# Optimization experiments

Hardware: AMD Instinct MI355X
Metric: run time of the kernel (lower is better)

The kernel has to match this reference:

```python
import jax, jax.numpy as jnp
import numpy as np

N, E, H, R, A = 100000, 1600000, 128, 500, 16  # nodes, edges, hidden, reservoir, actions
LN_EPS = 1e-5

def setup_inputs() -> dict:
    key = jax.random.key(0)
    ks = jax.random.split(key, 8)
    return {
        "node_feats": jax.random.normal(ks[0], (N, 2), jnp.float32),
        "edge_index": jax.random.randint(ks[1], (2, E), 0, N, dtype=jnp.int32),
        "esn_state": jax.random.normal(ks[2], (1, R), jnp.float32),
        "gcn_w": jax.random.normal(ks[3], (2, H), jnp.float32) * 0.5,
        "gcn_b": jnp.zeros((H,), jnp.float32),
        "ln_w": jnp.ones((H,), jnp.float32),
        "ln_b": jnp.zeros((H,), jnp.float32),
        "fc1_w": jax.random.normal(ks[4], (H + R, H), jnp.float32) * 0.04,
        "fc1_b": jnp.zeros((H,), jnp.float32),
        "fc2_w": jax.random.normal(ks[5], (H, A), jnp.float32) * 0.08,
        "fc2_b": jnp.zeros((A,), jnp.float32),
    }

def reference(node_feats, edge_index, esn_state, gcn_w, gcn_b, ln_w, ln_b,
              fc1_w, fc1_b, fc2_w, fc2_b):
    src, dst = edge_index[0], edge_index[1]
    n = node_feats.shape[0]
    # GCNConv: linear transform, then symmetric-normalized aggregation with self-loops
    h = node_feats @ gcn_w  # [N, H]
    deg = jax.ops.segment_sum(jnp.ones_like(src, dtype=h.dtype), dst, num_segments=n) + 1.0
    dis = jax.lax.rsqrt(deg)  # deg >= 1 due to self-loops
    norm = dis[src] * dis[dst]  # [E]
    agg = jax.ops.segment_sum(h[src] * norm[:, None], dst, num_segments=n)  # [N, H]
    x = agg + h * (dis * dis)[:, None] + gcn_b  # self-loop term + bias
    x = jax.nn.relu(x)
    # PyG LayerNorm, mode='graph', batch=None: normalize over all nodes & channels
    x = x - x.mean()
    x = x / (jnp.sqrt(x.var()) + LN_EPS)
    x = x * ln_w + ln_b
    pooled = x.sum(axis=0, keepdims=True)  # global_add_pool, single graph -> [1, H]
    z = jnp.concatenate([pooled, esn_state], axis=1)  # [1, H+R]
    z = jax.nn.relu(z @ fc1_w + fc1_b)
    logits = z @ fc2_w + fc2_b  # [1, A]
    return jax.nn.log_softmax(logits, axis=1)
```

## Files before the change

kernel.cpp:

```cpp
#include <hip/hip_runtime.h>
#include <math.h>

#define NN 100000
#define EE 1600000
#define HH 128
#define RR 500
#define AA 16
#define LN_EPS 1e-5f

#define BSH 8
#define NPB 256
#define NB 391
#define MAXPB 4608
#define EPW 8192
#define SCT 512
#define NWG_SC ((EE + EPW - 1) / EPW)
#define NZW 16
#define BAT 512
#define NSREP 8
#define NTW 16

__global__ __launch_bounds__(256) void k_init_esn(unsigned int* __restrict__ zero_region,
                                                  const float* __restrict__ esn,
                                                  const float* __restrict__ fc1_w,
                                                  float* __restrict__ zpart) {
    const int w = blockIdx.x, t = threadIdx.x;
    if (w == 0) {
        for (int j = t; j < 1544; j += 256) zero_region[j] = 0u;
        return;
    }
    const int sl = w - 1;
    const int k0 = sl * 32;
    const int k1 = min(k0 + 32, RR);
    if (t < HH) {
        float acc = 0.f;
        for (int k = k0; k < k1; ++k)
            acc = fmaf(esn[k], fc1_w[(size_t)(HH + k) * HH + t], acc);
        zpart[(size_t)sl * HH + t] = acc;
    }
}

__global__ __launch_bounds__(SCT) void k_scatter(const int* __restrict__ src,
                                                 const int* __restrict__ dst,
                                                 unsigned int* __restrict__ gctr,
                                                 unsigned int* __restrict__ payload) {
    __shared__ unsigned int rank[512], hbase[512];
    const int t = threadIdx.x;
    rank[t] = 0u; hbase[t] = 0u;
    __syncthreads();
    const int e0 = blockIdx.x * EPW;
    const int ecnt = max(0, min(EPW, EE - e0));
    const int nv = ecnt >> 2;
    const int4* d4 = reinterpret_cast<const int4*>(dst + e0);
    const int4* s4 = reinterpret_cast<const int4*>(src + e0);

    unsigned int pw[16], pbr[16];
    bool vk[4];

    #pragma unroll
    for (int kk = 0; kk < 4; ++kk) {
        const int k = t + kk * SCT;
        vk[kk] = (k < nv);
        if (vk[kk]) {
            int4 d = d4[k];
            int4 s = s4[k];
            #define GRAB(i, SS, DD) { \
                unsigned int dd = (unsigned)(DD), ss = (unsigned)(SS); \
                unsigned int b = dd >> BSH; \
                unsigned int r = atomicAdd(&rank[b], 1u); \
                pw[kk * 4 + i]  = (ss << BSH) | (dd & (NPB - 1)); \
                pbr[kk * 4 + i] = (b << 16) | (r & 0xFFFFu); }
            GRAB(0, s.x, d.x) GRAB(1, s.y, d.y) GRAB(2, s.z, d.z) GRAB(3, s.w, d.w)
            #undef GRAB
        }
    }
    __syncthreads();

    if (t < NB && rank[t] > 0u) hbase[t] = atomicAdd(&gctr[t], rank[t]);
    __syncthreads();

    #pragma unroll
    for (int kk = 0; kk < 4; ++kk) {
        if (vk[kk]) {
            #define PUT(i) { \
                unsigned int b = pbr[kk * 4 + i] >> 16; \
                unsigned int slot = hbase[b] + (pbr[kk * 4 + i] & 0xFFFFu); \
                if (slot < MAXPB) payload[(size_t)b * MAXPB + slot] = pw[kk * 4 + i]; }
            PUT(0) PUT(1) PUT(2) PUT(3)
            #undef PUT
        }
    }
}

__global__ __launch_bounds__(1024) void k_bdeg_g(const unsigned int* __restrict__ gctr,
                                                 const unsigned int* __restrict__ payload,
                                                 const float* __restrict__ nf,
                                                 float* __restrict__ rsv, float* __restrict__ g) {
    __shared__ unsigned int hist[NPB];
    const int b = blockIdx.x, t = threadIdx.x;
    if (t < NPB) hist[t] = 0u;
    __syncthreads();
    const unsigned int cnt = min(gctr[b], (unsigned int)MAXPB);
    const unsigned int* pl = payload + (size_t)b * MAXPB;
    const uint4* pl4 = reinterpret_cast<const uint4*>(pl);
    const unsigned int nv = cnt >> 2;
    for (unsigned int k = t; k < nv; k += 1024) {
        uint4 p = pl4[k];
        atomicAdd(&hist[p.x & (NPB - 1)], 1u);
        atomicAdd(&hist[p.y & (NPB - 1)], 1u);
        atomicAdd(&hist[p.z & (NPB - 1)], 1u);
        atomicAdd(&hist[p.w & (NPB - 1)], 1u);
    }
    for (unsigned int k = (nv << 2) + t; k < cnt; k += 1024)
        atomicAdd(&hist[pl[k] & (NPB - 1)], 1u);
    __syncthreads();
    if (t < NPB) {
        int node = (b << BSH) + t;
        if (node < NN) {
            float df = 1.0f + (float)hist[t];
            float rs = rsqrtf(df);
            rsv[node] = rs;
            float2 f = *reinterpret_cast<const float2*>(&nf[2 * node]);
            float2 gv; gv.x = rs * f.x; gv.y = rs * f.y;
            *reinterpret_cast<float2*>(&g[2 * node]) = gv;
        }
    }
}

__global__ __launch_bounds__(BAT) void k_bagg_node(const unsigned int* __restrict__ gctr,
        const unsigned int* __restrict__ payload,
        const float* __restrict__ g, const float* __restrict__ rsv,
        const float* __restrict__ gcn_w, const float* __restrict__ gcn_b,
        float* __restrict__ S8, float* __restrict__ T2_8) {
    __shared__ float agg[NPB * 2];
    __shared__ float shSf[HH];
    __shared__ float shw[8];
    const int b = blockIdx.x, t = threadIdx.x;
    agg[t] = 0.f;
    if (t < HH) shSf[t] = 0.f;
    __syncthreads();
    const unsigned int cnt = min(gctr[b], (unsigned int)MAXPB);
    const unsigned int* pl = payload + (size_t)b * MAXPB;
    const uint4* pl4 = reinterpret_cast<const uint4*>(pl);
    const unsigned int nv = cnt >> 2;

    #define ACC(P) { \
        unsigned int s_ = (P) >> BSH, dl_ = (P) & (NPB - 1); \
        float2 gv_ = *reinterpret_cast<const float2*>(&g[2 * s_]); \
        atomicAdd(&agg[dl_],       gv_.x); \
        atomicAdd(&agg[NPB + dl_], gv_.y); }

    {
        const unsigned int k1 = t, k2 = t + BAT;
        uint4 p1, p2;
        const bool v1 = k1 < nv, v2 = k2 < nv;
        if (v1) p1 = pl4[k1];
        if (v2) p2 = pl4[k2];
        if (v1) { ACC(p1.x) ACC(p1.y) ACC(p1.z) ACC(p1.w) }
        if (v2) { ACC(p2.x) ACC(p2.y) ACC(p2.z) ACC(p2.w) }
    }
    for (unsigned int k = t + 2 * BAT; k < nv; k += BAT) {
        uint4 p = pl4[k];
        ACC(p.x) ACC(p.y) ACC(p.z) ACC(p.w)
    }
    for (unsigned int k = (nv << 2) + t; k < cnt; k += BAT) {
        unsigned int p = pl[k];
        ACC(p)
    }
    #undef ACC
    __syncthreads();

    const int nvalid = min(NPB, NN - (b << BSH));
    if (t < nvalid) {
        int node = (b << BSH) + t;
        float rs = rsv[node];
        float2 gv = *reinterpret_cast<const float2*>(&g[2 * node]);
        agg[t]       = rs * (agg[t]       + gv.x);
        agg[NPB + t] = rs * (agg[NPB + t] + gv.y);
    }
    __syncthreads();

    const int ch = t & (HH - 1), slot = t >> 7;
    const float w0 = gcn_w[ch], w1 = gcn_w[HH + ch], bb = gcn_b[ch];
    float accS = 0.f, accT2 = 0.f;
    for (int j = slot; j < nvalid; j += 4) {
        float x = fmaf(agg[j], w0, fmaf(agg[NPB + j], w1, bb));
        float r = fmaxf(x, 0.f);
        accS  += r;
        accT2 += r * r;
    }
    atomicAdd(&shSf[ch], accS);
    float v = accT2;
    for (int o = 32; o; o >>= 1) v += __shfl_down(v, o, 64);
    if ((t & 63) == 0) shw[t >> 6] = v;
    __syncthreads();
    const int rep = b & (NSREP - 1);
    if (t < HH) atomicAdd(&S8[rep * HH + t], shSf[t]);
    if (t == 0) {
        float s2 = 0.f;
        #pragma unroll
        for (int w = 0; w < 8; ++w) s2 += shw[w];
        atomicAdd(&T2_8[rep], s2);
    }
}

__global__ __launch_bounds__(128) void k_tail1(const float* __restrict__ S8,
                                               const float* __restrict__ ln_w,
                                               const float* __restrict__ ln_b,
                                               const float* __restrict__ fc1_w,
                                               float* __restrict__ upart,
                                               float* __restrict__ c1part,
                                               float* __restrict__ c2part) {
    const int i = blockIdx.x, t = threadIdx.x;
    __shared__ float sh_sw[8], sh_lw[8], sh_lb[8];
    if (t < 8) {
        const int k = i * 8 + t;
        float s = 0.f;
        #pragma unroll
        for (int r = 0; r < NSREP; ++r) s += S8[r * HH + k];
        float lw = ln_w[k];
        sh_sw[t] = lw * s;
        sh_lw[t] = lw;
        sh_lb[t] = ln_b[k];
    }
    __syncthreads();
    float u = 0.f, c1 = 0.f, c2 = 0.f;
    #pragma unroll
    for (int kk = 0; kk < 8; ++kk) {
        float w = fc1_w[(size_t)(i * 8 + kk) * HH + t];
        u  = fmaf(sh_sw[kk], w, u);
        c1 = fmaf(sh_lw[kk], w, c1);
        c2 = fmaf(sh_lb[kk], w, c2);
    }
    upart[(size_t)i * HH + t]  = u;
    c1part[(size_t)i * HH + t] = c1;
    c2part[(size_t)i * HH + t] = c2;
}

__global__ __launch_bounds__(128) void k_tail2(const float* __restrict__ S8,
                                               const float* __restrict__ T2_8,
                                               const float* __restrict__ upart,
                                               const float* __restrict__ c1part,
                                               const float* __restrict__ c2part,
                                               const float* __restrict__ zpart,
                                               const float* __restrict__ fc1_b,
                                               const float* __restrict__ fc2_w,
                                               const float* __restrict__ fc2_b,
                                               float* __restrict__ out) {
    const int t = threadIdx.x;
    __shared__ float sh_z[HH], sh_logits[AA], shred[2], sh_t2[8];

    float s = 0.f;
    #pragma unroll
    for (int r = 0; r < NSREP; ++r) s += S8[r * HH + t];
    float vv = s;
    for (int o = 32; o; o >>= 1) vv += __shfl_down(vv, o, 64);
    if ((t & 63) == 0) shred[t >> 6] = vv;
    if (t < 8) sh_t2[t] = T2_8[t];
    __syncthreads();

    const float T1 = shred[0] + shred[1];
    float T2v = 0.f;
    #pragma unroll
    for (int r = 0; r < 8; ++r) T2v += sh_t2[r];
    const float cntf = (float)NN * (float)HH;
    const float mean = T1 / cntf;
    const float var  = T2v / cntf - mean * mean;
    const float denom = sqrtf(var) + LN_EPS;
    const float inv_denom = 1.0f / denom;
    const float nmean = (float)NN * mean;

    float u = 0.f, c1 = 0.f, c2 = 0.f, zs = 0.f;
    #pragma unroll
    for (int i = 0; i < NTW; ++i) {
        u  += upart[(size_t)i * HH + t];
        c1 += c1part[(size_t)i * HH + t];
        c2 += c2part[(size_t)i * HH + t];
        zs += zpart[(size_t)i * HH + t];
    }
    float fc1p = (u - nmean * c1) * inv_denom + (float)NN * c2;
    sh_z[t] = fmaxf(fc1p + zs + fc1_b[t], 0.f);
    __syncthreads();

    if (t < AA) {
        float l = fc2_b[t];
        for (int j = 0; j < HH; ++j)
            l = fmaf(sh_z[j], fc2_w[j * AA + t], l);
        sh_logits[t] = l;
    }
    __syncthreads();

    if (t == 0) {
        float m = sh_logits[0];
        for (int a = 1; a < AA; ++a) m = fmaxf(m, sh_logits[a]);
        float sum = 0.f;
        for (int a = 0; a < AA; ++a) sum += expf(sh_logits[a] - m);
        float lse = m + logf(sum);
        for (int a = 0; a < AA; ++a) out[a] = sh_logits[a] - lse;
    }
}


__global__ void k_initf(unsigned int* __restrict__ p, int n) {
    int i = blockIdx.x * blockDim.x + threadIdx.x;
    int stride = gridDim.x * blockDim.x;
    for (int j = i; j < n; j += stride) p[j] = 0u;
}

__global__ void k_deg1(const int* __restrict__ dst, int* __restrict__ deg, int e) {
    int i = blockIdx.x * blockDim.x + threadIdx.x;
    if (i < e) atomicAdd(&deg[dst[i]], 1);
}

__global__ void k_g1(const int* __restrict__ deg, const float* __restrict__ nf,
                     float* __restrict__ degf, float* __restrict__ g, int n) {
    int i = blockIdx.x * blockDim.x + threadIdx.x;
    if (i < n) {
        float df = (float)(1 + deg[i]);
        degf[i] = df;
        float rs = rsqrtf(df);
        float2 f = *reinterpret_cast<const float2*>(&nf[2 * i]);
        float2 gv; gv.x = rs * f.x; gv.y = rs * f.y;
        *reinterpret_cast<float2*>(&g[2 * i]) = gv;
    }
}

__global__ void k_edge1(const int* __restrict__ src, const int* __restrict__ dst,
                        const float* __restrict__ g, float* __restrict__ B, int e) {
    int i = blockIdx.x * blockDim.x + threadIdx.x;
    if (i < e) {
        int s = src[i], d = dst[i];
        float2 gv = *reinterpret_cast<const float2*>(&g[2 * s]);
        atomicAdd(&B[2 * d],     gv.x);
        atomicAdd(&B[2 * d + 1], gv.y);
    }
}

__global__ void k_node(const float* __restrict__ nf, const float* __restrict__ degf,
                       const float* __restrict__ B,
                       const float* __restrict__ gcn_w, const float* __restrict__ gcn_b,
                       float* __restrict__ S, float* __restrict__ T2, int n) {
    const int ch   = threadIdx.x & (HH - 1);
    const int slot = threadIdx.x >> 7;
    const float w0 = gcn_w[ch];
    const float w1 = gcn_w[HH + ch];
    const float b  = gcn_b[ch];
    float accS = 0.f, accT2 = 0.f;
    for (int i = blockIdx.x * 2 + slot; i < n; i += gridDim.x * 2) {
        float df   = degf[i];
        float invd = 1.0f / df;
        float rs   = rsqrtf(df);
        float2 bv = *reinterpret_cast<const float2*>(&B[2 * i]);
        float2 f  = *reinterpret_cast<const float2*>(&nf[2 * i]);
        float b0 = rs * bv.x + f.x * invd;
        float b1 = rs * bv.y + f.y * invd;
        float xv = fmaf(b0, w0, fmaf(b1, w1, b));
        float r  = fmaxf(xv, 0.f);
        accS  += r;
        accT2 += r * r;
    }
    __shared__ float shS[HH];
    if (slot == 1) shS[ch] = accS;
    __syncthreads();
    if (slot == 0) atomicAdd(&S[ch], accS + shS[ch]);
    float v = accT2;
    for (int o = 32; o; o >>= 1) v += __shfl_down(v, o, 64);
    __shared__ float shw[4];
    if ((threadIdx.x & 63) == 0) shw[threadIdx.x >> 6] = v;
    __syncthreads();
    if (threadIdx.x == 0) atomicAdd(T2, shw[0] + shw[1] + shw[2] + shw[3]);
}

__global__ void k_final(const float* __restrict__ S, const float* __restrict__ T2ptr,
                        const float* __restrict__ esn,
                        const float* __restrict__ ln_w, const float* __restrict__ ln_b,
                        const float* __restrict__ fc1_w, const float* __restrict__ fc1_b,
                        const float* __restrict__ fc2_w, const float* __restrict__ fc2_b,
                        float* __restrict__ out) {
    const int t = threadIdx.x;
    __shared__ float sh_pooled[HH];
    __shared__ float sh_z[HH];
    __shared__ float sh_logits[AA];
    __shared__ float shred[2];

    float s = S[t];
    float v = s;
    for (int o = 32; o; o >>= 1) v += __shfl_down(v, o, 64);
    if ((t & 63) == 0) shred[t >> 6] = v;
    __syncthreads();
    const float T1 = shred[0] + shred[1];
    const float T2 = *T2ptr;
    const float cnt = (float)NN * (float)HH;
    const float mean = T1 / cnt;
    const float var  = T2 / cnt - mean * mean;
    const float denom = sqrtf(var) + LN_EPS;
    sh_pooled[t] = ln_w[t] * (s - (float)NN * mean) / denom + (float)NN * ln_b[t];
    __syncthreads();

    float acc = fc1_b[t];
    for (int k = 0; k < HH; ++k)
        acc = fmaf(sh_pooled[k], fc1_w[k * HH + t], acc);
    for (int k = 0; k < RR; ++k)
        acc = fmaf(esn[k], fc1_w[(HH + k) * HH + t], acc);
    sh_z[t] = fmaxf(acc, 0.f);
    __syncthreads();

    if (t < AA) {
        float l = fc2_b[t];
        for (int j = 0; j < HH; ++j)
            l = fmaf(sh_z[j], fc2_w[j * AA + t], l);
        sh_logits[t] = l;
    }
    __syncthreads();

    if (t == 0) {
        float m = sh_logits[0];
        for (int a = 1; a < AA; ++a) m = fmaxf(m, sh_logits[a]);
        float sum = 0.f;
        for (int a = 0; a < AA; ++a) sum += expf(sh_logits[a] - m);
        float lse = m + logf(sum);
        for (int a = 0; a < AA; ++a) out[a] = sh_logits[a] - lse;
    }
}

extern "C" void kernel_launch(void* const* d_in, const int* in_sizes, int n_in,
                              void* d_out, int out_size, void* d_ws, size_t ws_size,
                              hipStream_t stream) {
    const float* nf     = (const float*)d_in[0];
    const int*   ei     = (const int*)d_in[1];
    const float* esn    = (const float*)d_in[2];
    const float* gcn_w  = (const float*)d_in[3];
    const float* gcn_b  = (const float*)d_in[4];
    const float* ln_w   = (const float*)d_in[5];
    const float* ln_b   = (const float*)d_in[6];
    const float* fc1_w  = (const float*)d_in[7];
    const float* fc1_b  = (const float*)d_in[8];
    const float* fc2_w  = (const float*)d_in[9];
    const float* fc2_b  = (const float*)d_in[10];
    float* out = (float*)d_out;
    float* ws  = (float*)d_ws;

    const size_t OFF_S8      = 512;
    const size_t OFF_T28     = OFF_S8 + NSREP * HH;
    const size_t OFF_UPART   = OFF_T28 + 8;
    const size_t OFF_C1      = OFF_UPART + (size_t)NTW * HH;
    const size_t OFF_C2      = OFF_C1 + (size_t)NTW * HH;
    const size_t OFF_ZPART   = OFF_C2 + (size_t)NTW * HH;
    const size_t OFF_PAYLOAD = OFF_ZPART + (size_t)NZW * HH;
    const size_t OFF_RSV     = OFF_PAYLOAD + (size_t)NB * MAXPB;
    const size_t OFF_G       = OFF_RSV + NN;
    const size_t NEED_BKT    = (OFF_G + 2 * (size_t)NN) * 4;

    if (ws_size >= NEED_BKT) {
        unsigned int* gctr    = (unsigned int*)ws;
        float*        S8      = ws + OFF_S8;
        float*        T2_8    = ws + OFF_T28;
        float*        upart   = ws + OFF_UPART;
        float*        c1part  = ws + OFF_C1;
        float*        c2part  = ws + OFF_C2;
        float*        zpart   = ws + OFF_ZPART;
        unsigned int* payload = (unsigned int*)ws + OFF_PAYLOAD;
        float*        rsv     = ws + OFF_RSV;
        float*        g       = ws + OFF_G;

        hipLaunchKernelGGL(k_init_esn,  dim3(NZW + 1), dim3(256),  0, stream,
                           (unsigned int*)ws, esn, fc1_w, zpart);
        hipLaunchKernelGGL(k_scatter,   dim3(NWG_SC),  dim3(SCT),  0, stream, ei, ei + EE, gctr, payload);
        hipLaunchKernelGGL(k_bdeg_g,    dim3(NB),      dim3(1024), 0, stream, gctr, payload, nf, rsv, g);
        hipLaunchKernelGGL(k_bagg_node, dim3(NB),      dim3(BAT),  0, stream,
                           gctr, payload, g, rsv, gcn_w, gcn_b, S8, T2_8);
        hipLaunchKernelGGL(k_tail1,     dim3(NTW),     dim3(128),  0, stream,
                           S8, ln_w, ln_b, fc1_w, upart, c1part, c2part);
        hipLaunchKernelGGL(k_tail2,     dim3(1),       dim3(128),  0, stream,
                           S8, T2_8, upart, c1part, c2part, zpart, fc1_b, fc2_w, fc2_b, out);
    } else {
        int*   deg  = (int*)ws;
        float* B    = ws + NN;
        float* S    = ws + 3 * (size_t)NN;
        float* T2   = ws + 3 * (size_t)NN + 128;
        float* degf = ws + 3 * (size_t)NN + 130;
        float* g    = ws + 4 * (size_t)NN + 130;
        const int eb = (EE + 255) / 256;
        const int nb = (NN + 255) / 256;
        hipLaunchKernelGGL(k_initf, dim3(2048), dim3(256), 0, stream, (unsigned int*)ws, 3 * NN + 129);
        hipLaunchKernelGGL(k_deg1,  dim3(eb),   dim3(256), 0, stream, ei + EE, deg, EE);
        hipLaunchKernelGGL(k_g1,    dim3(nb),   dim3(256), 0, stream, deg, nf, degf, g, NN);
        hipLaunchKernelGGL(k_edge1, dim3(eb),   dim3(256), 0, stream, ei, ei + EE, g, B, EE);
        hipLaunchKernelGGL(k_node,  dim3(512),  dim3(256), 0, stream, nf, degf, B, gcn_w, gcn_b, S, T2, NN);
        hipLaunchKernelGGL(k_final, dim3(1),    dim3(128), 0, stream,
                           S, T2, esn, ln_w, ln_b, fc1_w, fc1_b, fc2_w, fc2_b, out);
    }
}
```

Before: 68.74 us.

## Counting-sort bucket edges into per-node CSR and gather without LDS atomics

The degree kernel now records each edge's rank within its destination histogram, runs a shared-memory prefix scan, and writes source indices sorted by destination into a second payload buffer, along with per-node start and length. The aggregation kernel then assigns one thread per node, which sums its neighbours' features sequentially in registers. This replaces the shared-memory float atomics in aggregation. In exchange it adds an extra global write and read of the sorted payload, and each thread's serial gather loop is exposed to load imbalance across nodes and to memory latency.

```diff
diff --git a/kernel.cpp b/kernel.cpp
--- a/kernel.cpp
+++ b/kernel.cpp
@@ -16,7 +16,6 @@
 #define SCT 512
 #define NWG_SC ((EE + EPW - 1) / EPW)
 #define NZW 16
-#define BAT 512
 #define NSREP 8
 #define NTW 16
 
@@ -93,10 +92,12 @@
 }
 
 __global__ __launch_bounds__(1024) void k_bdeg_g(const unsigned int* __restrict__ gctr,
-                                                 const unsigned int* __restrict__ payload,
-                                                 const float* __restrict__ nf,
-                                                 float* __restrict__ rsv, float* __restrict__ g) {
+        const unsigned int* __restrict__ payload,
+        const float* __restrict__ nf,
+        float* __restrict__ rsv, float* __restrict__ g,
+        unsigned int* __restrict__ payload2, unsigned int* __restrict__ sstart) {
     __shared__ unsigned int hist[NPB];
+    __shared__ unsigned int start[NPB];
     const int b = blockIdx.x, t = threadIdx.x;
     if (t < NPB) hist[t] = 0u;
     __syncthreads();
@@ -104,17 +105,62 @@
     const unsigned int* pl = payload + (size_t)b * MAXPB;
     const uint4* pl4 = reinterpret_cast<const uint4*>(pl);
     const unsigned int nv = cnt >> 2;
-    for (unsigned int k = t; k < nv; k += 1024) {
-        uint4 p = pl4[k];
-        atomicAdd(&hist[p.x & (NPB - 1)], 1u);
-        atomicAdd(&hist[p.y & (NPB - 1)], 1u);
-        atomicAdd(&hist[p.z & (NPB - 1)], 1u);
-        atomicAdd(&hist[p.w & (NPB - 1)], 1u);
-    }
-    for (unsigned int k = (nv << 2) + t; k < cnt; k += 1024)
-        atomicAdd(&hist[pl[k] & (NPB - 1)], 1u);
-    __syncthreads();
+
+    uint4 pv0, pv1;
+    unsigned int rk0[4], rk1[4];
+    const bool v0 = (unsigned)t < nv;
+    const bool v1 = (unsigned)(t + 1024) < nv;
+    if (v0) {
+        pv0 = pl4[t];
+        rk0[0] = atomicAdd(&hist[pv0.x & (NPB - 1)], 1u);
+        rk0[1] = atomicAdd(&hist[pv0.y & (NPB - 1)], 1u);
+        rk0[2] = atomicAdd(&hist[pv0.z & (NPB - 1)], 1u);
+        rk0[3] = atomicAdd(&hist[pv0.w & (NPB - 1)], 1u);
+    }
+    if (v1) {
+        pv1 = pl4[t + 1024];
+        rk1[0] = atomicAdd(&hist[pv1.x & (NPB - 1)], 1u);
+        rk1[1] = atomicAdd(&hist[pv1.y & (NPB - 1)], 1u);
+        rk1[2] = atomicAdd(&hist[pv1.z & (NPB - 1)], 1u);
+        rk1[3] = atomicAdd(&hist[pv1.w & (NPB - 1)], 1u);
+    }
+    unsigned int tp = 0u, tr = 0u;
+    const bool vt = (unsigned)t < (cnt & 3u);
+    if (vt) {
+        tp = pl[(nv << 2) + t];
+        tr = atomicAdd(&hist[tp & (NPB - 1)], 1u);
+    }
+    __syncthreads();
+
+    if (t < NPB) start[t] = hist[t];
+    __syncthreads();
+    for (int off = 1; off < NPB; off <<= 1) {
+        unsigned int v = 0u;
+        if (t < NPB && t >= off) v = start[t - off];
+        __syncthreads();
+        if (t < NPB) start[t] += v;
+        __syncthreads();
+    }
+    if (t < NPB) start[t] -= hist[t];
+    __syncthreads();
+
+    unsigned int* p2 = payload2 + (size_t)b * MAXPB;
+    if (v0) {
+        p2[start[pv0.x & (NPB - 1)] + rk0[0]] = pv0.x >> BSH;
+        p2[start[pv0.y & (NPB - 1)] + rk0[1]] = pv0.y >> BSH;
+        p2[start[pv0.z & (NPB - 1)] + rk0[2]] = pv0.z >> BSH;
+        p2[start[pv0.w & (NPB - 1)] + rk0[3]] = pv0.w >> BSH;
+    }
+    if (v1) {
+        p2[start[pv1.x & (NPB - 1)] + rk1[0]] = pv1.x >> BSH;
+        p2[start[pv1.y & (NPB - 1)] + rk1[1]] = pv1.y >> BSH;
+        p2[start[pv1.z & (NPB - 1)] + rk1[2]] = pv1.z >> BSH;
+        p2[start[pv1.w & (NPB - 1)] + rk1[3]] = pv1.w >> BSH;
+    }
+    if (vt) p2[start[tp & (NPB - 1)] + tr] = tp >> BSH;
+
     if (t < NPB) {
+        sstart[(size_t)b * NPB + t] = (start[t] << 16) | (hist[t] & 0xFFFFu);
         int node = (b << BSH) + t;
         if (node < NN) {
             float df = 1.0f + (float)hist[t];
@@ -127,63 +173,45 @@
     }
 }
 
-__global__ __launch_bounds__(BAT) void k_bagg_node(const unsigned int* __restrict__ gctr,
-        const unsigned int* __restrict__ payload,
+__global__ __launch_bounds__(256) void k_bagg_node(const unsigned int* __restrict__ payload2,
+        const unsigned int* __restrict__ sstart,
         const float* __restrict__ g, const float* __restrict__ rsv,
         const float* __restrict__ gcn_w, const float* __restrict__ gcn_b,
         float* __restrict__ S8, float* __restrict__ T2_8) {
     __shared__ float agg[NPB * 2];
     __shared__ float shSf[HH];
-    __shared__ float shw[8];
+    __shared__ float shw[4];
     const int b = blockIdx.x, t = threadIdx.x;
-    agg[t] = 0.f;
     if (t < HH) shSf[t] = 0.f;
-    __syncthreads();
-    const unsigned int cnt = min(gctr[b], (unsigned int)MAXPB);
-    const unsigned int* pl = payload + (size_t)b * MAXPB;
-    const uint4* pl4 = reinterpret_cast<const uint4*>(pl);
-    const unsigned int nv = cnt >> 2;
-
-    #define ACC(P) { \
-        unsigned int s_ = (P) >> BSH, dl_ = (P) & (NPB - 1); \
-        float2 gv_ = *reinterpret_cast<const float2*>(&g[2 * s_]); \
-        atomicAdd(&agg[dl_],       gv_.x); \
-        atomicAdd(&agg[NPB + dl_], gv_.y); }
-
-    {
-        const unsigned int k1 = t, k2 = t + BAT;
-        uint4 p1, p2;
-        const bool v1 = k1 < nv, v2 = k2 < nv;
-        if (v1) p1 = pl4[k1];
-        if (v2) p2 = pl4[k2];
-        if (v1) { ACC(p1.x) ACC(p1.y) ACC(p1.z) ACC(p1.w) }
-        if (v2) { ACC(p2.x) ACC(p2.y) ACC(p2.z) ACC(p2.w) }
-    }
-    for (unsigned int k = t + 2 * BAT; k < nv; k += BAT) {
-        uint4 p = pl4[k];
-        ACC(p.x) ACC(p.y) ACC(p.z) ACC(p.w)
-    }
-    for (unsigned int k = (nv << 2) + t; k < cnt; k += BAT) {
-        unsigned int p = pl[k];
-        ACC(p)
-    }
-    #undef ACC
-    __syncthreads();
 
     const int nvalid = min(NPB, NN - (b << BSH));
+    const unsigned int* p2 = payload2 + (size_t)b * MAXPB;
+
+    float ax = 0.f, ay = 0.f;
     if (t < nvalid) {
+        unsigned int sl = sstart[(size_t)b * NPB + t];
+        unsigned int s0 = sl >> 16, len = sl & 0xFFFFu;
+        #pragma unroll 4
+        for (unsigned int k = 0; k < len; ++k) {
+            unsigned int s = p2[s0 + k];
+            float2 gv = *reinterpret_cast<const float2*>(&g[2 * s]);
+            ax += gv.x; ay += gv.y;
+        }
         int node = (b << BSH) + t;
         float rs = rsv[node];
         float2 gv = *reinterpret_cast<const float2*>(&g[2 * node]);
-        agg[t]       = rs * (agg[t]       + gv.x);
-        agg[NPB + t] = rs * (agg[NPB + t] + gv.y);
+        agg[t]       = rs * (ax + gv.x);
+        agg[NPB + t] = rs * (ay + gv.y);
+    } else {
+        agg[t]       = 0.f;
+        agg[NPB + t] = 0.f;
     }
     __syncthreads();
 
     const int ch = t & (HH - 1), slot = t >> 7;
     const float w0 = gcn_w[ch], w1 = gcn_w[HH + ch], bb = gcn_b[ch];
     float accS = 0.f, accT2 = 0.f;
-    for (int j = slot; j < nvalid; j += 4) {
+    for (int j = slot; j < nvalid; j += 2) {
         float x = fmaf(agg[j], w0, fmaf(agg[NPB + j], w1, bb));
         float r = fmaxf(x, 0.f);
         accS  += r;
@@ -199,7 +227,7 @@
     if (t == 0) {
         float s2 = 0.f;
         #pragma unroll
-        for (int w = 0; w < 8; ++w) s2 += shw[w];
+        for (int w = 0; w < 4; ++w) s2 += shw[w];
         atomicAdd(&T2_8[rep], s2);
     }
 }
@@ -440,35 +468,40 @@
     float* out = (float*)d_out;
     float* ws  = (float*)d_ws;
 
-    const size_t OFF_S8      = 512;
-    const size_t OFF_T28     = OFF_S8 + NSREP * HH;
-    const size_t OFF_UPART   = OFF_T28 + 8;
-    const size_t OFF_C1      = OFF_UPART + (size_t)NTW * HH;
-    const size_t OFF_C2      = OFF_C1 + (size_t)NTW * HH;
-    const size_t OFF_ZPART   = OFF_C2 + (size_t)NTW * HH;
-    const size_t OFF_PAYLOAD = OFF_ZPART + (size_t)NZW * HH;
-    const size_t OFF_RSV     = OFF_PAYLOAD + (size_t)NB * MAXPB;
-    const size_t OFF_G       = OFF_RSV + NN;
-    const size_t NEED_BKT    = (OFF_G + 2 * (size_t)NN) * 4;
+    const size_t OFF_S8       = 512;
+    const size_t OFF_T28      = OFF_S8 + NSREP * HH;
+    const size_t OFF_UPART    = OFF_T28 + 8;
+    const size_t OFF_C1       = OFF_UPART + (size_t)NTW * HH;
+    const size_t OFF_C2       = OFF_C1 + (size_t)NTW * HH;
+    const size_t OFF_ZPART    = OFF_C2 + (size_t)NTW * HH;
+    const size_t OFF_SSTART   = OFF_ZPART + (size_t)NZW * HH;
+    const size_t OFF_PAYLOAD  = OFF_SSTART + (size_t)NB * NPB;
+    const size_t OFF_PAYLOAD2 = OFF_PAYLOAD + (size_t)NB * MAXPB;
+    const size_t OFF_RSV      = OFF_PAYLOAD2 + (size_t)NB * MAXPB;
+    const size_t OFF_G        = OFF_RSV + NN;
+    const size_t NEED_BKT     = (OFF_G + 2 * (size_t)NN) * 4;
 
     if (ws_size >= NEED_BKT) {
-        unsigned int* gctr    = (unsigned int*)ws;
-        float*        S8      = ws + OFF_S8;
-        float*        T2_8    = ws + OFF_T28;
-        float*        upart   = ws + OFF_UPART;
-        float*        c1part  = ws + OFF_C1;
-        float*        c2part  = ws + OFF_C2;
-        float*        zpart   = ws + OFF_ZPART;
-        unsigned int* payload = (unsigned int*)ws + OFF_PAYLOAD;
-        float*        rsv     = ws + OFF_RSV;
-        float*        g       = ws + OFF_G;
+        unsigned int* gctr     = (unsigned int*)ws;
+        float*        S8       = ws + OFF_S8;
+        float*        T2_8     = ws + OFF_T28;
+        float*        upart    = ws + OFF_UPART;
+        float*        c1part   = ws + OFF_C1;
+        float*        c2part   = ws + OFF_C2;
+        float*        zpart    = ws + OFF_ZPART;
+        unsigned int* sstart   = (unsigned int*)ws + OFF_SSTART;
+        unsigned int* payload  = (unsigned int*)ws + OFF_PAYLOAD;
+        unsigned int* payload2 = (unsigned int*)ws + OFF_PAYLOAD2;
+        float*        rsv      = ws + OFF_RSV;
+        float*        g        = ws + OFF_G;
 
         hipLaunchKernelGGL(k_init_esn,  dim3(NZW + 1), dim3(256),  0, stream,
                            (unsigned int*)ws, esn, fc1_w, zpart);
         hipLaunchKernelGGL(k_scatter,   dim3(NWG_SC),  dim3(SCT),  0, stream, ei, ei + EE, gctr, payload);
-        hipLaunchKernelGGL(k_bdeg_g,    dim3(NB),      dim3(1024), 0, stream, gctr, payload, nf, rsv, g);
-        hipLaunchKernelGGL(k_bagg_node, dim3(NB),      dim3(BAT),  0, stream,
-                           gctr, payload, g, rsv, gcn_w, gcn_b, S8, T2_8);
+        hipLaunchKernelGGL(k_bdeg_g,    dim3(NB),      dim3(1024), 0, stream,
+                           gctr, payload, nf, rsv, g, payload2, sstart);
+        hipLaunchKernelGGL(k_bagg_node, dim3(NB),      dim3(256),  0, stream,
+                           payload2, sstart, g, rsv, gcn_w, gcn_b, S8, T2_8);
         hipLaunchKernelGGL(k_tail1,     dim3(NTW),     dim3(128),  0, stream,
                            S8, ln_w, ln_b, fc1_w, upart, c1part, c2part);
         hipLaunchKernelGGL(k_tail2,     dim3(1),       dim3(128),  0, stream,
```

Result: no change. 69.68 us (+1.4%).
